# Optimization experiments

Measured on AMD Instinct MI355X. Metric: run time of the kernel, lower is better.

Reference implementation:

```python
import jax, jax.numpy as jnp
import numpy as np

N_NODES = 50000
N_EDGES = 800000
VOCAB = 1000
EMBED = 128
HIDDEN = 128
N_CLASSES = 10
N_GRAPHS = 64


def setup_inputs() -> dict:
    key = jax.random.key(0)
    ks = jax.random.split(key, 12)
    x_idx = jax.random.randint(ks[0], (N_NODES,), 0, VOCAB)
    edge_index = jax.random.randint(ks[1], (2, N_EDGES), 0, N_NODES)
    batch = jnp.sort(jax.random.randint(ks[2], (N_NODES,), 0, N_GRAPHS))
    s = lambda k, shp, fan: jax.random.normal(k, shp, jnp.float32) / jnp.sqrt(fan)
    return {
        "x_idx": x_idx,
        "edge_index": edge_index,
        "batch": batch,
        "embed_table": jax.random.normal(ks[3], (VOCAB, EMBED), jnp.float32),
        "Wl1": s(ks[4], (HIDDEN, EMBED), EMBED),
        "bl1": jnp.zeros((HIDDEN,), jnp.float32),
        "Wr1": s(ks[5], (HIDDEN, EMBED), EMBED),
        "Wl2": s(ks[6], (HIDDEN, HIDDEN), HIDDEN),
        "bl2": jnp.zeros((HIDDEN,), jnp.float32),
        "Wr2": s(ks[7], (HIDDEN, HIDDEN), HIDDEN),
        "linW": s(ks[8], (N_CLASSES, HIDDEN), HIDDEN),
        "linb": jnp.zeros((N_CLASSES,), jnp.float32),
    }


def _sage_conv(x, src, dst, Wl, bl, Wr):
    # mean aggregation of source features into destination nodes (PyG SAGEConv, aggr='mean')
    msg_sum = jax.ops.segment_sum(x[src], dst, num_segments=N_NODES)  # [N, d]
    cnt = jax.ops.segment_sum(jnp.ones((src.shape[0],), x.dtype), dst, num_segments=N_NODES)
    agg = msg_sum / jnp.maximum(cnt, 1.0)[:, None]
    # out = lin_l(agg) + lin_r(x); lin_l has bias, lin_r has none
    return agg @ Wl.T + bl + x @ Wr.T


def reference(x_idx, edge_index, batch, embed_table, Wl1, bl1, Wr1, Wl2, bl2, Wr2, linW, linb):
    src, dst = edge_index[0], edge_index[1]
    x = embed_table[x_idx]  # [N, EMBED]
    x = jax.nn.relu(_sage_conv(x, src, dst, Wl1, bl1, Wr1))
    x = jax.nn.relu(_sage_conv(x, src, dst, Wl2, bl2, Wr2))
    # global mean pool over graphs
    g_sum = jax.ops.segment_sum(x, batch, num_segments=N_GRAPHS)  # [G, HIDDEN]
    g_cnt = jax.ops.segment_sum(jnp.ones((x.shape[0],), x.dtype), batch, num_segments=N_GRAPHS)
    pooled = g_sum / jnp.maximum(g_cnt, 1.0)[:, None]
    return pooled @ linW.T + linb  # [G, N_CLASSES]
```

## Files before the change

kernel.cpp:

```cpp
#include <hip/hip_runtime.h>

#define N_NODES 50000
#define N_EDGES 800000
#define N_GRAPHS 64
#define SCAN_BLOCKS 196

#define NCHUNK 32
#define CHUNK_E (N_EDGES / NCHUNK)
#define NRANGE 4
#define RSZ (N_NODES / NRANGE)

#define K1_HIST (NCHUNK * NRANGE)
#define K1_EMBED (N_NODES * 16 / 256)
#define K1_PREP 32

typedef __bf16 bf16x8 __attribute__((ext_vector_type(8)));
typedef float f32x4 __attribute__((ext_vector_type(4)));

static __device__ __forceinline__ unsigned short f2bf(float f) {
    union { float f; unsigned u; } v; v.f = f;
    unsigned u = v.u;
    u += 0x7fffu + ((u >> 16) & 1u);
    return (unsigned short)(u >> 16);
}
static __device__ __forceinline__ float bflo(unsigned w) {
    union { unsigned u; float f; } v; v.u = w << 16; return v.f;
}
static __device__ __forceinline__ float bfhi(unsigned w) {
    union { unsigned u; float f; } v; v.u = w & 0xffff0000u; return v.f;
}

#define ACC8(A, v) do { \
    A[0] += bflo((v).x); A[1] += bfhi((v).x); \
    A[2] += bflo((v).y); A[3] += bfhi((v).y); \
    A[4] += bflo((v).z); A[5] += bfhi((v).z); \
    A[6] += bflo((v).w); A[7] += bfhi((v).w); } while (0)

__global__ __launch_bounds__(256) void k1_kernel(const int* __restrict__ dst,
                                                 int* __restrict__ part,
                                                 const int* __restrict__ x_idx,
                                                 const float* __restrict__ table,
                                                 unsigned short* __restrict__ X,
                                                 const float* __restrict__ Wl1,
                                                 const float* __restrict__ Wr1,
                                                 const float* __restrict__ Wl2,
                                                 const float* __restrict__ Wr2,
                                                 unsigned short* __restrict__ blob,
                                                 float* __restrict__ gsum) {
    const int b = blockIdx.x;
    if (b < K1_HIST) {
        __shared__ int h[RSZ];
        const int c = b >> 2;
        const int r = b & 3;
        const int rbase = r * RSZ;
        for (int i = threadIdx.x; i < RSZ; i += 256) h[i] = 0;
        __syncthreads();
        const int4* d4 = (const int4*)(dst + c * CHUNK_E);
        for (int i = threadIdx.x; i < CHUNK_E / 4; i += 256) {
            int4 d = d4[i];
            unsigned a;
            a = (unsigned)(d.x - rbase); if (a < RSZ) atomicAdd(&h[a], 1);
            a = (unsigned)(d.y - rbase); if (a < RSZ) atomicAdd(&h[a], 1);
            a = (unsigned)(d.z - rbase); if (a < RSZ) atomicAdd(&h[a], 1);
            a = (unsigned)(d.w - rbase); if (a < RSZ) atomicAdd(&h[a], 1);
        }
        __syncthreads();
        int* p = part + (size_t)c * N_NODES + rbase;
        for (int i = threadIdx.x; i < RSZ; i += 256) p[i] = h[i];
    } else if (b < K1_HIST + K1_EMBED) {
        int i = (b - K1_HIST) * 256 + threadIdx.x;
        int n = i >> 4, cq = i & 15;
        const float4* src = (const float4*)(table + (size_t)x_idx[n] * 128 + cq * 8);
        float4 a = src[0], bb = src[1];
        uint4 o;
        o.x = (unsigned)f2bf(a.x)  | ((unsigned)f2bf(a.y)  << 16);
        o.y = (unsigned)f2bf(a.z)  | ((unsigned)f2bf(a.w)  << 16);
        o.z = (unsigned)f2bf(bb.x) | ((unsigned)f2bf(bb.y) << 16);
        o.w = (unsigned)f2bf(bb.z) | ((unsigned)f2bf(bb.w) << 16);
        ((uint4*)X)[i] = o;
    } else {
        int s = (b - K1_HIST - K1_EMBED) * 256 + threadIdx.x;
        gsum[s] = 0.f;
        int g = s >> 12;
        int sl = s & 4095;
        int fidx = sl >> 6, lane = sl & 63;
        int m = fidx >> 5, kk = (fidx >> 3) & 3, tile = fidx & 7;
        const float* W = g ? (m ? Wr2 : Wl2) : (m ? Wr1 : Wl1);
        int n  = tile * 16 + (lane & 15);
        int k0 = kk * 32 + (lane >> 4) * 8;
        const float4* src = (const float4*)(W + n * 128 + k0);
        float4 a = src[0], bb = src[1];
        uint4 o;
        o.x = (unsigned)f2bf(a.x)  | ((unsigned)f2bf(a.y)  << 16);
        o.y = (unsigned)f2bf(a.z)  | ((unsigned)f2bf(a.w)  << 16);
        o.z = (unsigned)f2bf(bb.x) | ((unsigned)f2bf(bb.y) << 16);
        o.w = (unsigned)f2bf(bb.z) | ((unsigned)f2bf(bb.w) << 16);
        ((uint4*)blob)[s] = o;
    }
}

__global__ __launch_bounds__(256) void cntsum_kernel(const int* __restrict__ part,
                                                     int* __restrict__ cnt,
                                                     int* __restrict__ bsum) {
    int t = threadIdx.x;
    int n = blockIdx.x * 256 + t;
    int s = 0;
    if (n < N_NODES) {
#pragma unroll
        for (int c = 0; c < NCHUNK; ++c) s += part[(size_t)c * N_NODES + n];
        cnt[n] = s;
    }
#pragma unroll
    for (int off = 32; off > 0; off >>= 1) s += __shfl_down(s, off, 64);
    __shared__ int ws[4];
    if ((t & 63) == 0) ws[t >> 6] = s;
    __syncthreads();
    if (t == 0) bsum[blockIdx.x] = ws[0] + ws[1] + ws[2] + ws[3];
}

__global__ __launch_bounds__(256) void rowptroff_kernel(const int* __restrict__ cnt,
                                                        const int* __restrict__ bsum,
                                                        const int* __restrict__ part,
                                                        int* __restrict__ rowptr,
                                                        int* __restrict__ off) {
    __shared__ int sb[256];
    __shared__ int sd[256];
    int t = threadIdx.x;
    sb[t] = (t < SCAN_BLOCKS) ? bsum[t] : 0;
    __syncthreads();
    for (int o = 1; o < 256; o <<= 1) {
        int add = (t >= o) ? sb[t - o] : 0;
        __syncthreads();
        sb[t] += add;
        __syncthreads();
    }
    int boff = (blockIdx.x > 0) ? sb[blockIdx.x - 1] : 0;

    int i = blockIdx.x * 256 + t;
    int v = (i < N_NODES) ? cnt[i] : 0;
    sd[t] = v;
    __syncthreads();
    for (int o = 1; o < 256; o <<= 1) {
        int add = (t >= o) ? sd[t - o] : 0;
        __syncthreads();
        sd[t] += add;
        __syncthreads();
    }
    int excl = sd[t] - v + boff;
    if (i < N_NODES) {
        rowptr[i] = excl;
        if (i == N_NODES - 1) rowptr[N_NODES] = excl + v;
        int run = excl;
#pragma unroll
        for (int c = 0; c < NCHUNK; ++c) {
            off[(size_t)c * N_NODES + i] = run;
            run += part[(size_t)c * N_NODES + i];
        }
    }
}

__global__ __launch_bounds__(256) void scatter_kernel(const int* __restrict__ src,
                                                      const int* __restrict__ dst,
                                                      const int* __restrict__ off,
                                                      int* __restrict__ csr) {
    __shared__ int h[RSZ];
    const int c = blockIdx.x >> 2;
    const int r = blockIdx.x & 3;
    const int rbase = r * RSZ;
    const int* o = off + (size_t)c * N_NODES + rbase;
    for (int i = threadIdx.x; i < RSZ; i += 256) h[i] = o[i];
    __syncthreads();
    const int4* d4 = (const int4*)(dst + c * CHUNK_E);
    const int4* s4 = (const int4*)(src + c * CHUNK_E);
    for (int i = threadIdx.x; i < CHUNK_E / 4; i += 256) {
        int4 d = d4[i];
        int4 s = s4[i];
        unsigned a;
        a = (unsigned)(d.x - rbase); if (a < RSZ) csr[atomicAdd(&h[a], 1)] = s.x;
        a = (unsigned)(d.y - rbase); if (a < RSZ) csr[atomicAdd(&h[a], 1)] = s.y;
        a = (unsigned)(d.z - rbase); if (a < RSZ) csr[atomicAdd(&h[a], 1)] = s.z;
        a = (unsigned)(d.w - rbase); if (a < RSZ) csr[atomicAdd(&h[a], 1)] = s.w;
    }
}

__global__ __launch_bounds__(256) void agg_kernel(const unsigned short* __restrict__ X,
                                                  const int* __restrict__ rowptr,
                                                  const int* __restrict__ csr,
                                                  unsigned short* __restrict__ AGG) {
    const int t = threadIdx.x;
    const int lane = t & 63;
    const int e = lane >> 4;
    const int f = lane & 15;
    const int n = blockIdx.x * 4 + (t >> 6);
    const int beg = rowptr[n], end = rowptr[n + 1];
    const char* Xb = (const char*)X + f * 16;
    float a[8];
#pragma unroll
    for (int k = 0; k < 8; ++k) a[k] = 0.f;

    int i = beg;
    for (; i + 8 <= end; i += 8) {
        int c0 = csr[i + e];
        int c1 = csr[i + 4 + e];
        uint4 v0 = *(const uint4*)(Xb + (size_t)c0 * 256);
        uint4 v1 = *(const uint4*)(Xb + (size_t)c1 * 256);
        ACC8(a, v0);
        ACC8(a, v1);
    }
    if (i + 4 <= end) {
        int c0 = csr[i + e];
        uint4 v0 = *(const uint4*)(Xb + (size_t)c0 * 256);
        ACC8(a, v0);
        i += 4;
    }
    if (i + e < end) {
        int c0 = csr[i + e];
        uint4 v0 = *(const uint4*)(Xb + (size_t)c0 * 256);
        ACC8(a, v0);
    }

#pragma unroll
    for (int k = 0; k < 8; ++k) {
        a[k] += __shfl_xor(a[k], 16, 64);
        a[k] += __shfl_xor(a[k], 32, 64);
    }

    if (e == 0) {
        float inv = 1.f / (float)max(end - beg, 1);
        uint4 o;
        o.x = (unsigned)f2bf(a[0] * inv) | ((unsigned)f2bf(a[1] * inv) << 16);
        o.y = (unsigned)f2bf(a[2] * inv) | ((unsigned)f2bf(a[3] * inv) << 16);
        o.z = (unsigned)f2bf(a[4] * inv) | ((unsigned)f2bf(a[5] * inv) << 16);
        o.w = (unsigned)f2bf(a[6] * inv) | ((unsigned)f2bf(a[7] * inv) << 16);
        *(uint4*)((char*)AGG + (size_t)n * 256 + f * 16) = o;
    }
}

__global__ __launch_bounds__(256) void gemm_kernel(const unsigned short* __restrict__ A0,
                                                   const unsigned short* __restrict__ A1,
                                                   const unsigned short* __restrict__ wblob,
                                                   const float* __restrict__ bias,
                                                   unsigned short* __restrict__ Y) {
    __shared__ char lds[65536];
    const int t = threadIdx.x, lane = t & 63, w = t >> 6;

    {
        const char* src = (const char*)wblob + w * 16384 + lane * 16;
        char* dst = lds + w * 16384;
#pragma unroll
        for (int i = 0; i < 16; ++i) {
            __builtin_amdgcn_global_load_lds(
                (const __attribute__((address_space(1))) unsigned*)(src + i * 1024),
                (__attribute__((address_space(3))) unsigned*)(dst + i * 1024), 16, 0, 0);
        }
    }
    __syncthreads();

    const int kl = (lane >> 4) * 8;
    const int c     = lane & 15;
    const int rbase = (lane >> 4) * 4;

#pragma unroll 1
    for (int tt = 0; tt < 2; ++tt) {
        const int tile0 = blockIdx.x * 2 + tt;
        if (tile0 * 128 >= N_NODES) break;
        const int row0 = tile0 * 128 + w * 32;

        f32x4 acc[2][8];
#pragma unroll
        for (int rt = 0; rt < 2; ++rt)
#pragma unroll
            for (int tl = 0; tl < 8; ++tl) acc[rt][tl] = (f32x4){0.f, 0.f, 0.f, 0.f};

        int rA = min(row0 + (lane & 15),      N_NODES - 1);
        int rB = min(row0 + 16 + (lane & 15), N_NODES - 1);

#pragma unroll
        for (int km = 0; km < 8; ++km) {
            const unsigned short* A = (km < 4) ? A0 : A1;
            int k0 = (km & 3) * 32 + kl;
            bf16x8 a0 = *(const bf16x8*)(A + (size_t)rA * 128 + k0);
            bf16x8 a1 = *(const bf16x8*)(A + (size_t)rB * 128 + k0);
            const char* bbase = lds + km * 8192 + lane * 16;
#pragma unroll
            for (int tile = 0; tile < 8; ++tile) {
                bf16x8 b = *(const bf16x8*)(bbase + tile * 1024);
                acc[0][tile] = __builtin_amdgcn_mfma_f32_16x16x32_bf16(a0, b, acc[0][tile], 0, 0, 0);
                acc[1][tile] = __builtin_amdgcn_mfma_f32_16x16x32_bf16(a1, b, acc[1][tile], 0, 0, 0);
            }
        }

#pragma unroll
        for (int rt = 0; rt < 2; ++rt) {
#pragma unroll
            for (int tile = 0; tile < 8; ++tile) {
                int col = tile * 16 + c;
                float bv = bias[col];
#pragma unroll
                for (int j = 0; j < 4; ++j) {
                    int r = row0 + rt * 16 + rbase + j;
                    if (r < N_NODES)
                        Y[(size_t)r * 128 + col] = f2bf(fmaxf(acc[rt][tile][j] + bv, 0.f));
                }
            }
        }
    }
}

__global__ __launch_bounds__(256) void gemm_pool_kernel(const unsigned short* __restrict__ A0,
                                                        const unsigned short* __restrict__ A1,
                                                        const unsigned short* __restrict__ wblob,
                                                        const float* __restrict__ bias,
                                                        const int* __restrict__ batch,
                                                        float* __restrict__ gsum) {
    __shared__ char lds[65536];
    const int t = threadIdx.x, lane = t & 63, w = t >> 6;
    const int brow0 = blockIdx.x * 128;
    const int row0  = brow0 + w * 32;

    {
        const char* src = (const char*)wblob + w * 16384 + lane * 16;
        char* dst = lds + w * 16384;
#pragma unroll
        for (int i = 0; i < 16; ++i) {
            __builtin_amdgcn_global_load_lds(
                (const __attribute__((address_space(1))) unsigned*)(src + i * 1024),
                (__attribute__((address_space(3))) unsigned*)(dst + i * 1024), 16, 0, 0);
        }
    }
    __syncthreads();

    f32x4 acc[2][8];
#pragma unroll
    for (int rt = 0; rt < 2; ++rt)
#pragma unroll
        for (int tl = 0; tl < 8; ++tl) acc[rt][tl] = (f32x4){0.f, 0.f, 0.f, 0.f};

    int rA = min(row0 + (lane & 15),      N_NODES - 1);
    int rB = min(row0 + 16 + (lane & 15), N_NODES - 1);
    const int kl = (lane >> 4) * 8;

#pragma unroll
    for (int km = 0; km < 8; ++km) {
        const unsigned short* A = (km < 4) ? A0 : A1;
        int k0 = (km & 3) * 32 + kl;
        bf16x8 a0 = *(const bf16x8*)(A + (size_t)rA * 128 + k0);
        bf16x8 a1 = *(const bf16x8*)(A + (size_t)rB * 128 + k0);
        const char* bbase = lds + km * 8192 + lane * 16;
#pragma unroll
        for (int tile = 0; tile < 8; ++tile) {
            bf16x8 b = *(const bf16x8*)(bbase + tile * 1024);
            acc[0][tile] = __builtin_amdgcn_mfma_f32_16x16x32_bf16(a0, b, acc[0][tile], 0, 0, 0);
            acc[1][tile] = __builtin_amdgcn_mfma_f32_16x16x32_bf16(a1, b, acc[1][tile], 0, 0, 0);
        }
    }

    __syncthreads();
    float* ftile = (float*)lds;
    const int c     = lane & 15;
    const int rbase = (lane >> 4) * 4;
#pragma unroll
    for (int rt = 0; rt < 2; ++rt) {
#pragma unroll
        for (int tile = 0; tile < 8; ++tile) {
            int col = tile * 16 + c;
            float bv = bias[col];
#pragma unroll
            for (int j = 0; j < 4; ++j) {
                int lr = w * 32 + rt * 16 + rbase + j;
                ftile[lr * 128 + col] = fmaxf(acc[rt][tile][j] + bv, 0.f);
            }
        }
    }
    __syncthreads();

    const int col  = t & 127;
    const int half = t >> 7;
    float s = 0.f;
    int curg = -1;
    for (int rr = 0; rr < 64; ++rr) {
        int r = brow0 + half * 64 + rr;
        if (r >= N_NODES) break;
        int g = batch[r];
        if (g != curg) {
            if (curg >= 0) atomicAdd(&gsum[curg * 128 + col], s);
            curg = g; s = 0.f;
        }
        s += ftile[(half * 64 + rr) * 128 + col];
    }
    if (curg >= 0) atomicAdd(&gsum[curg * 128 + col], s);
}

__global__ void final_kernel(const float* __restrict__ gsum, const int* __restrict__ batch,
                             const float* __restrict__ linW, const float* __restrict__ linb,
                             float* __restrict__ out) {
    int t = blockIdx.x * 256 + threadIdx.x;
    if (t >= N_GRAPHS * 10) return;
    int g = t / 10, j = t % 10;
    int bnd[2];
    for (int c = 0; c < 2; ++c) {
        int target = g + c;
        int lo = 0, hi = N_NODES;
        while (lo < hi) { int mid = (lo + hi) >> 1; if (batch[mid] < target) lo = mid + 1; else hi = mid; }
        bnd[c] = lo;
    }
    float invc = 1.f / (float)max(bnd[1] - bnd[0], 1);
    float s = 0.f;
    for (int k = 0; k < 128; ++k) s += gsum[g * 128 + k] * linW[j * 128 + k];
    out[t] = linb[j] + s * invc;
}

extern "C" void kernel_launch(void* const* d_in, const int* in_sizes, int n_in,
                              void* d_out, int out_size, void* d_ws, size_t ws_size,
                              hipStream_t stream) {
    const int*   x_idx = (const int*)d_in[0];
    const int*   eidx  = (const int*)d_in[1];
    const int*   batch = (const int*)d_in[2];
    const float* table = (const float*)d_in[3];
    const float* Wl1   = (const float*)d_in[4];
    const float* bl1   = (const float*)d_in[5];
    const float* Wr1   = (const float*)d_in[6];
    const float* Wl2   = (const float*)d_in[7];
    const float* bl2   = (const float*)d_in[8];
    const float* Wr2   = (const float*)d_in[9];
    const float* linW  = (const float*)d_in[10];
    const float* linb  = (const float*)d_in[11];
    float*       out   = (float*)d_out;

    const int* src = eidx;
    const int* dst = eidx + N_EDGES;

    unsigned short* X    = (unsigned short*)d_ws;
    unsigned short* AGG  = X   + (size_t)N_NODES * 128;
    unsigned short* Y1   = AGG + (size_t)N_NODES * 128;
    unsigned short* blob = Y1  + (size_t)N_NODES * 128;
    float* gsum = (float*)(blob + 65536);
    int* cnt    = (int*)(gsum + N_GRAPHS * 128);
    int* rowptr = cnt + N_NODES;
    int* csr    = rowptr + (N_NODES + 1);
    int* bsum   = csr + N_EDGES;
    int* part   = bsum + SCAN_BLOCKS;
    int* off    = part + (size_t)NCHUNK * N_NODES;

    k1_kernel<<<K1_HIST + K1_EMBED + K1_PREP, 256, 0, stream>>>(
        dst, part, x_idx, table, X, Wl1, Wr1, Wl2, Wr2, blob, gsum);
    cntsum_kernel   <<<SCAN_BLOCKS, 256, 0, stream>>>(part, cnt, bsum);
    rowptroff_kernel<<<SCAN_BLOCKS, 256, 0, stream>>>(cnt, bsum, part, rowptr, off);
    scatter_kernel  <<<NCHUNK * NRANGE, 256, 0, stream>>>(src, dst, off, csr);

    agg_kernel <<<dim3(N_NODES / 4), 256, 0, stream>>>(X, rowptr, csr, AGG);
    gemm_kernel<<<dim3((N_NODES + 255) / 256), 256, 0, stream>>>(AGG, X, blob, bl1, Y1);
    agg_kernel      <<<dim3(N_NODES / 4), 256, 0, stream>>>(Y1, rowptr, csr, AGG);
    gemm_pool_kernel<<<dim3((N_NODES + 127) / 128), 256, 0, stream>>>(AGG, Y1, blob + 32768, bl2, batch, gsum);

    final_kernel<<<3, 256, 0, stream>>>(gsum, batch, linW, linb, out);
}
```

Measured before the change: 161.6 us.

## Gather layer-1 neighbors from bf16 vocab table and give each node a 16-lane group

Adds a bf16 copy of the 1000-row embedding table, built in k1, and a new first-layer aggregation kernel. That kernel gathers neighbor features through x_idx from this small table, which stays cache-resident, instead of from the 50000-node X array. Both aggregation kernels now give each 16-lane group its own node, unrolled over 8 edges, which removes the cross-lane shuffle reduction. The cost is an extra dependent x_idx load per edge, and more load imbalance across lanes because node degrees differ.

```diff
diff --git a/kernel.cpp b/kernel.cpp
--- a/kernel.cpp
+++ b/kernel.cpp
@@ -3,6 +3,7 @@
 #define N_NODES 50000
 #define N_EDGES 800000
 #define N_GRAPHS 64
+#define VOCAB 1000
 #define SCAN_BLOCKS 196
 
 #define NCHUNK 32
@@ -12,6 +13,7 @@
 
 #define K1_HIST (NCHUNK * NRANGE)
 #define K1_EMBED (N_NODES * 16 / 256)
+#define K1_TBL 63
 #define K1_PREP 32
 
 typedef __bf16 bf16x8 __attribute__((ext_vector_type(8)));
@@ -36,11 +38,21 @@
     A[4] += bflo((v).z); A[5] += bfhi((v).z); \
     A[6] += bflo((v).w); A[7] += bfhi((v).w); } while (0)
 
+static __device__ __forceinline__ uint4 cvt2x4(float4 a, float4 b) {
+    uint4 o;
+    o.x = (unsigned)f2bf(a.x) | ((unsigned)f2bf(a.y) << 16);
+    o.y = (unsigned)f2bf(a.z) | ((unsigned)f2bf(a.w) << 16);
+    o.z = (unsigned)f2bf(b.x) | ((unsigned)f2bf(b.y) << 16);
+    o.w = (unsigned)f2bf(b.z) | ((unsigned)f2bf(b.w) << 16);
+    return o;
+}
+
 __global__ __launch_bounds__(256) void k1_kernel(const int* __restrict__ dst,
                                                  int* __restrict__ part,
                                                  const int* __restrict__ x_idx,
                                                  const float* __restrict__ table,
                                                  unsigned short* __restrict__ X,
+                                                 unsigned short* __restrict__ TBL,
                                                  const float* __restrict__ Wl1,
                                                  const float* __restrict__ Wr1,
                                                  const float* __restrict__ Wl2,
@@ -71,15 +83,15 @@
         int i = (b - K1_HIST) * 256 + threadIdx.x;
         int n = i >> 4, cq = i & 15;
         const float4* src = (const float4*)(table + (size_t)x_idx[n] * 128 + cq * 8);
-        float4 a = src[0], bb = src[1];
-        uint4 o;
-        o.x = (unsigned)f2bf(a.x)  | ((unsigned)f2bf(a.y)  << 16);
-        o.y = (unsigned)f2bf(a.z)  | ((unsigned)f2bf(a.w)  << 16);
-        o.z = (unsigned)f2bf(bb.x) | ((unsigned)f2bf(bb.y) << 16);
-        o.w = (unsigned)f2bf(bb.z) | ((unsigned)f2bf(bb.w) << 16);
-        ((uint4*)X)[i] = o;
+        ((uint4*)X)[i] = cvt2x4(src[0], src[1]);
+    } else if (b < K1_HIST + K1_EMBED + K1_TBL) {
+        int i = (b - K1_HIST - K1_EMBED) * 256 + threadIdx.x;
+        if (i < VOCAB * 16) {
+            const float4* src = (const float4*)(table + (size_t)(i >> 4) * 128 + (i & 15) * 8);
+            ((uint4*)TBL)[i] = cvt2x4(src[0], src[1]);
+        }
     } else {
-        int s = (b - K1_HIST - K1_EMBED) * 256 + threadIdx.x;
+        int s = (b - K1_HIST - K1_EMBED - K1_TBL) * 256 + threadIdx.x;
         gsum[s] = 0.f;
         int g = s >> 12;
         int sl = s & 4095;
@@ -89,13 +101,7 @@
         int n  = tile * 16 + (lane & 15);
         int k0 = kk * 32 + (lane >> 4) * 8;
         const float4* src = (const float4*)(W + n * 128 + k0);
-        float4 a = src[0], bb = src[1];
-        uint4 o;
-        o.x = (unsigned)f2bf(a.x)  | ((unsigned)f2bf(a.y)  << 16);
-        o.y = (unsigned)f2bf(a.z)  | ((unsigned)f2bf(a.w)  << 16);
-        o.z = (unsigned)f2bf(bb.x) | ((unsigned)f2bf(bb.y) << 16);
-        o.w = (unsigned)f2bf(bb.z) | ((unsigned)f2bf(bb.w) << 16);
-        ((uint4*)blob)[s] = o;
+        ((uint4*)blob)[s] = cvt2x4(src[0], src[1]);
     }
 }
 
@@ -183,57 +189,96 @@
     }
 }
 
+__global__ __launch_bounds__(256) void agg1_kernel(const unsigned short* __restrict__ TBL,
+                                                   const int* __restrict__ x_idx,
+                                                   const int* __restrict__ rowptr,
+                                                   const int* __restrict__ csr,
+                                                   unsigned short* __restrict__ AGG) {
+    const int t = threadIdx.x;
+    const int lane = t & 63;
+    const int f = lane & 15;
+    const int n = blockIdx.x * 16 + (t >> 6) * 4 + (lane >> 4);
+    int beg = rowptr[n], end = rowptr[n + 1];
+    const char* Tb = (const char*)TBL + f * 16;
+    float a[8];
+#pragma unroll
+    for (int k = 0; k < 8; ++k) a[k] = 0.f;
+    int i = beg;
+    for (; i + 8 <= end; i += 8) {
+        int r0 = x_idx[csr[i + 0]], r1 = x_idx[csr[i + 1]];
+        int r2 = x_idx[csr[i + 2]], r3 = x_idx[csr[i + 3]];
+        int r4 = x_idx[csr[i + 4]], r5 = x_idx[csr[i + 5]];
+        int r6 = x_idx[csr[i + 6]], r7 = x_idx[csr[i + 7]];
+        uint4 v0 = *(const uint4*)(Tb + (size_t)r0 * 256);
+        uint4 v1 = *(const uint4*)(Tb + (size_t)r1 * 256);
+        uint4 v2 = *(const uint4*)(Tb + (size_t)r2 * 256);
+        uint4 v3 = *(const uint4*)(Tb + (size_t)r3 * 256);
+        uint4 v4 = *(const uint4*)(Tb + (size_t)r4 * 256);
+        uint4 v5 = *(const uint4*)(Tb + (size_t)r5 * 256);
+        uint4 v6 = *(const uint4*)(Tb + (size_t)r6 * 256);
+        uint4 v7 = *(const uint4*)(Tb + (size_t)r7 * 256);
+        ACC8(a, v0); ACC8(a, v1); ACC8(a, v2); ACC8(a, v3);
+        ACC8(a, v4); ACC8(a, v5); ACC8(a, v6); ACC8(a, v7);
+    }
+    for (; i < end; ++i) {
+        int r0 = x_idx[csr[i]];
+        uint4 v0 = *(const uint4*)(Tb + (size_t)r0 * 256);
+        ACC8(a, v0);
+    }
+    float inv = 1.f / (float)max(end - beg, 1);
+    uint4 o;
+    o.x = (unsigned)f2bf(a[0] * inv) | ((unsigned)f2bf(a[1] * inv) << 16);
+    o.y = (unsigned)f2bf(a[2] * inv) | ((unsigned)f2bf(a[3] * inv) << 16);
+    o.z = (unsigned)f2bf(a[4] * inv) | ((unsigned)f2bf(a[5] * inv) << 16);
+    o.w = (unsigned)f2bf(a[6] * inv) | ((unsigned)f2bf(a[7] * inv) << 16);
+    *(uint4*)((char*)AGG + (size_t)n * 256 + f * 16) = o;
+}
+
 __global__ __launch_bounds__(256) void agg_kernel(const unsigned short* __restrict__ X,
                                                   const int* __restrict__ rowptr,
                                                   const int* __restrict__ csr,
                                                   unsigned short* __restrict__ AGG) {
     const int t = threadIdx.x;
     const int lane = t & 63;
-    const int e = lane >> 4;
     const int f = lane & 15;
-    const int n = blockIdx.x * 4 + (t >> 6);
-    const int beg = rowptr[n], end = rowptr[n + 1];
+    const int n = blockIdx.x * 16 + (t >> 6) * 4 + (lane >> 4);
+    int beg = rowptr[n], end = rowptr[n + 1];
     const char* Xb = (const char*)X + f * 16;
     float a[8];
 #pragma unroll
     for (int k = 0; k < 8; ++k) a[k] = 0.f;
-
     int i = beg;
     for (; i + 8 <= end; i += 8) {
-        int c0 = csr[i + e];
-        int c1 = csr[i + 4 + e];
-        uint4 v0 = *(const uint4*)(Xb + (size_t)c0 * 256);
-        uint4 v1 = *(const uint4*)(Xb + (size_t)c1 * 256);
+        int s0 = csr[i + 0], s1 = csr[i + 1], s2 = csr[i + 2], s3 = csr[i + 3];
+        int s4 = csr[i + 4], s5 = csr[i + 5], s6 = csr[i + 6], s7 = csr[i + 7];
+        uint4 v0 = *(const uint4*)(Xb + (size_t)s0 * 256);
+        uint4 v1 = *(const uint4*)(Xb + (size_t)s1 * 256);
+        uint4 v2 = *(const uint4*)(Xb + (size_t)s2 * 256);
+        uint4 v3 = *(const uint4*)(Xb + (size_t)s3 * 256);
+        uint4 v4 = *(const uint4*)(Xb + (size_t)s4 * 256);
+        uint4 v5 = *(const uint4*)(Xb + (size_t)s5 * 256);
+        uint4 v6 = *(const uint4*)(Xb + (size_t)s6 * 256);
+        uint4 v7 = *(const uint4*)(Xb + (size_t)s7 * 256);
+        ACC8(a, v0); ACC8(a, v1); ACC8(a, v2); ACC8(a, v3);
+        ACC8(a, v4); ACC8(a, v5); ACC8(a, v6); ACC8(a, v7);
+    }
+    for (; i + 2 <= end; i += 2) {
+        int s0 = csr[i], s1 = csr[i + 1];
+        uint4 v0 = *(const uint4*)(Xb + (size_t)s0 * 256);
+        uint4 v1 = *(const uint4*)(Xb + (size_t)s1 * 256);
+        ACC8(a, v0); ACC8(a, v1);
+    }
+    if (i < end) {
+        uint4 v0 = *(const uint4*)(Xb + (size_t)csr[i] * 256);
         ACC8(a, v0);
-        ACC8(a, v1);
-    }
-    if (i + 4 <= end) {
-        int c0 = csr[i + e];
-        uint4 v0 = *(const uint4*)(Xb + (size_t)c0 * 256);
-        ACC8(a, v0);
-        i += 4;
-    }
-    if (i + e < end) {
-        int c0 = csr[i + e];
-        uint4 v0 = *(const uint4*)(Xb + (size_t)c0 * 256);
-        ACC8(a, v0);
-    }
-
-#pragma unroll
-    for (int k = 0; k < 8; ++k) {
-        a[k] += __shfl_xor(a[k], 16, 64);
-        a[k] += __shfl_xor(a[k], 32, 64);
-    }
-
-    if (e == 0) {
-        float inv = 1.f / (float)max(end - beg, 1);
-        uint4 o;
-        o.x = (unsigned)f2bf(a[0] * inv) | ((unsigned)f2bf(a[1] * inv) << 16);
-        o.y = (unsigned)f2bf(a[2] * inv) | ((unsigned)f2bf(a[3] * inv) << 16);
-        o.z = (unsigned)f2bf(a[4] * inv) | ((unsigned)f2bf(a[5] * inv) << 16);
-        o.w = (unsigned)f2bf(a[6] * inv) | ((unsigned)f2bf(a[7] * inv) << 16);
-        *(uint4*)((char*)AGG + (size_t)n * 256 + f * 16) = o;
-    }
+    }
+    float inv = 1.f / (float)max(end - beg, 1);
+    uint4 o;
+    o.x = (unsigned)f2bf(a[0] * inv) | ((unsigned)f2bf(a[1] * inv) << 16);
+    o.y = (unsigned)f2bf(a[2] * inv) | ((unsigned)f2bf(a[3] * inv) << 16);
+    o.z = (unsigned)f2bf(a[4] * inv) | ((unsigned)f2bf(a[5] * inv) << 16);
+    o.w = (unsigned)f2bf(a[6] * inv) | ((unsigned)f2bf(a[7] * inv) << 16);
+    *(uint4*)((char*)AGG + (size_t)n * 256 + f * 16) = o;
 }
 
 __global__ __launch_bounds__(256) void gemm_kernel(const unsigned short* __restrict__ A0,
@@ -434,7 +479,8 @@
     unsigned short* AGG  = X   + (size_t)N_NODES * 128;
     unsigned short* Y1   = AGG + (size_t)N_NODES * 128;
     unsigned short* blob = Y1  + (size_t)N_NODES * 128;
-    float* gsum = (float*)(blob + 65536);
+    unsigned short* TBL  = blob + 65536;
+    float* gsum = (float*)(TBL + VOCAB * 128);
     int* cnt    = (int*)(gsum + N_GRAPHS * 128);
     int* rowptr = cnt + N_NODES;
     int* csr    = rowptr + (N_NODES + 1);
@@ -442,15 +488,15 @@
     int* part   = bsum + SCAN_BLOCKS;
     int* off    = part + (size_t)NCHUNK * N_NODES;
 
-    k1_kernel<<<K1_HIST + K1_EMBED + K1_PREP, 256, 0, stream>>>(
-        dst, part, x_idx, table, X, Wl1, Wr1, Wl2, Wr2, blob, gsum);
+    k1_kernel<<<K1_HIST + K1_EMBED + K1_TBL + K1_PREP, 256, 0, stream>>>(
+        dst, part, x_idx, table, X, TBL, Wl1, Wr1, Wl2, Wr2, blob, gsum);
     cntsum_kernel   <<<SCAN_BLOCKS, 256, 0, stream>>>(part, cnt, bsum);
     rowptroff_kernel<<<SCAN_BLOCKS, 256, 0, stream>>>(cnt, bsum, part, rowptr, off);
     scatter_kernel  <<<NCHUNK * NRANGE, 256, 0, stream>>>(src, dst, off, csr);
 
-    agg_kernel <<<dim3(N_NODES / 4), 256, 0, stream>>>(X, rowptr, csr, AGG);
+    agg1_kernel<<<dim3(N_NODES / 16), 256, 0, stream>>>(TBL, x_idx, rowptr, csr, AGG);
     gemm_kernel<<<dim3((N_NODES + 255) / 256), 256, 0, stream>>>(AGG, X, blob, bl1, Y1);
-    agg_kernel      <<<dim3(N_NODES / 4), 256, 0, stream>>>(Y1, rowptr, csr, AGG);
+    agg_kernel      <<<dim3(N_NODES / 16), 256, 0, stream>>>(Y1, rowptr, csr, AGG);
     gemm_pool_kernel<<<dim3((N_NODES + 127) / 128), 256, 0, stream>>>(AGG, Y1, blob + 32768, bl2, batch, gsum);
 
     final_kernel<<<3, 256, 0, stream>>>(gsum, batch, linW, linb, out);
```

Measured after the change: 156.5 us. 1.03x faster.
